# Kernel optimization log

Measured on AMD Instinct MI355X. Metric: run time of the kernel, lower is better.

The kernel has to match this reference:

```python
import jax, jax.numpy as jnp
import numpy as np

D = 1024; NHEAD = 8; NQ = 256; B = 8; HM = 64; WM = 64; S = HM * WM; FF = 4 * D
EPS_LN = 1e-5


def _ln(x, g, b):
    m = x.mean(-1, keepdims=True)
    v = ((x - m) ** 2).mean(-1, keepdims=True)
    return (x - m) / jnp.sqrt(v + EPS_LN) * g + b


def _self_attn(x, w_in, b_in, w_out, b_out, nhead):
    # x: [L, B, D] (torch MultiheadAttention, batch_first=False, eval mode)
    L, Bn, Dm = x.shape
    hd = Dm // nhead
    qkv = x @ w_in.T + b_in  # [L, B, 3D]
    q, k, v = jnp.split(qkv, 3, axis=-1)
    sp = lambda t: t.reshape(L, Bn, nhead, hd).transpose(1, 2, 0, 3)  # [B, H, L, hd]
    q, k, v = sp(q), sp(k), sp(v)
    attn = jax.nn.softmax(jnp.einsum('bhqd,bhkd->bhqk', q, k) / float(hd) ** 0.5, axis=-1)
    out = jnp.einsum('bhqk,bhkd->bhqd', attn, v)
    out = out.transpose(2, 0, 1, 3).reshape(L, Bn, Dm)
    return out @ w_out.T + b_out


def setup_inputs() -> dict:
    key = jax.random.key(0)
    ks = iter(jax.random.split(key, 40))
    nrm = lambda shape: jax.random.normal(next(ks), shape, jnp.float32) * 0.02
    return dict(
        query=jax.random.normal(next(ks), (NQ, B, D), jnp.float32),
        memory=jax.random.normal(next(ks), (S, B, D), jnp.float32),
        prev_mask=jax.random.uniform(next(ks), (B, NQ, HM, WM), dtype=jnp.float32),
        h_mem=HM, w_mem=WM,
        sa_in_w=nrm((3 * D, D)), sa_in_b=jnp.zeros((3 * D,), jnp.float32),
        sa_out_w=nrm((D, D)), sa_out_b=jnp.zeros((D,), jnp.float32),
        ln1_g=jnp.ones((D,), jnp.float32), ln1_b=jnp.zeros((D,), jnp.float32),
        ln2_g=jnp.ones((D,), jnp.float32), ln2_b=jnp.zeros((D,), jnp.float32),
        ln3_g=jnp.ones((D,), jnp.float32), ln3_b=jnp.zeros((D,), jnp.float32),
        wq=nrm((D, D)), bq=jnp.zeros((D,), jnp.float32),
        wk=nrm((D, D)), bk=jnp.zeros((D,), jnp.float32),
        wv=nrm((D, D)), bv=jnp.zeros((D,), jnp.float32),
        wo=nrm((D, D)), bo=jnp.zeros((D,), jnp.float32),
        w1=nrm((FF, D)), b1=jnp.zeros((FF,), jnp.float32),
        w2=nrm((D, FF)), b2=jnp.zeros((D,), jnp.float32),
        mask_w=nrm((S, D)), mask_b=jnp.zeros((S,), jnp.float32),
    )


def reference(query, memory, prev_mask, h_mem, w_mem,
              sa_in_w, sa_in_b, sa_out_w, sa_out_b,
              ln1_g, ln1_b, ln2_g, ln2_b, ln3_g, ln3_b,
              wq, bq, wk, bk, wv, bv, wo, bo,
              w1, b1, w2, b2, mask_w, mask_b):
    nq, Bn, d_model = query.shape
    # --- self attention block ---
    q_norm = _ln(query, ln1_g, ln1_b)
    q2 = _self_attn(q_norm, sa_in_w, sa_in_b, sa_out_w, sa_out_b, NHEAD)
    query = query + q2
    # --- masked cross attention (single-head, as in source) ---
    Q = (_ln(query, ln2_g, ln2_b) @ wq.T + bq).transpose(1, 0, 2)  # [B, NQ, D]
    K = (memory @ wk.T + bk).transpose(1, 0, 2)                    # [B, S, D]
    V = (memory @ wv.T + bv).transpose(1, 0, 2)                    # [B, S, D]
    scores = jnp.einsum('bqd,bsd->bqs', Q, K) / float(d_model) ** 0.5
    scores = scores + jnp.log(prev_mask.reshape(Bn, nq, -1) + 1e-6)
    attn = jax.nn.softmax(scores, axis=-1)
    attn_out = jnp.einsum('bqs,bsd->bqd', attn, V).transpose(1, 0, 2)  # [NQ, B, D]
    query = query + (attn_out @ wo.T + bo)
    # --- FFN ---
    h = jax.nn.gelu(_ln(query, ln3_g, ln3_b) @ w1.T + b1, approximate=False)
    query = query + (h @ w2.T + b2)
    # --- mask prediction ---
    q_for_mask = query.transpose(1, 0, 2)                # [B, NQ, D]
    mask_logits = q_for_mask @ mask_w.T + mask_b          # [B, NQ, H*W]
    pred_mask = jax.nn.sigmoid(mask_logits.reshape(Bn, nq, h_mem, w_mem))
    return (query, pred_mask)
```

## Files before the change

kernel.cpp:

```cpp
#include <hip/hip_runtime.h>
#include <cstdint>


typedef __attribute__((ext_vector_type(8))) __bf16 bf16x8;
typedef __attribute__((ext_vector_type(4))) float f32x4;
typedef __attribute__((ext_vector_type(8))) unsigned short ushort8;
typedef __attribute__((ext_vector_type(4))) unsigned short ushort4v;

__device__ __forceinline__ unsigned short f2bf(float f) {
  return __builtin_bit_cast(unsigned short, (__bf16)f);
}

__global__ __launch_bounds__(256) void cast_bf16_kernel(const float* __restrict__ in,
                                                        unsigned short* __restrict__ out,
                                                        int n8) {
  int i = blockIdx.x * 256 + threadIdx.x;
  if (i >= n8) return;
  const float4* p = (const float4*)in + (size_t)i * 2;
  float4 a = p[0], b = p[1];
  ushort8 o;
  o[0] = f2bf(a.x); o[1] = f2bf(a.y); o[2] = f2bf(a.z); o[3] = f2bf(a.w);
  o[4] = f2bf(b.x); o[5] = f2bf(b.y); o[6] = f2bf(b.z); o[7] = f2bf(b.w);
  ((ushort8*)out)[i] = o;
}

struct CastSegs {
  const float* src[9];
  int cum[10];
};
__global__ __launch_bounds__(256) void cast_multi_kernel(CastSegs cs,
                                                         unsigned short* __restrict__ out) {
  int i = blockIdx.x * 256 + threadIdx.x;
  if (i >= cs.cum[9]) return;
  int s = 0;
  while (i >= cs.cum[s + 1]) s++;
  const float4* p = (const float4*)cs.src[s] + (size_t)(i - cs.cum[s]) * 2;
  float4 a = p[0], b = p[1];
  ushort8 o;
  o[0] = f2bf(a.x); o[1] = f2bf(a.y); o[2] = f2bf(a.z); o[3] = f2bf(a.w);
  o[4] = f2bf(b.x); o[5] = f2bf(b.y); o[6] = f2bf(b.z); o[7] = f2bf(b.w);
  ((ushort8*)out)[i] = o;
}

__global__ __launch_bounds__(256) void bias_concat_kernel(const float* __restrict__ a,
                                                          const float* __restrict__ b,
                                                          float* __restrict__ o) {
  int i = blockIdx.x * 256 + threadIdx.x;
  o[i] = i < 1024 ? a[i] : b[i - 1024];
}

__global__ __launch_bounds__(256) void ln_bf16_kernel(const float* __restrict__ x,
                                                      const float* __restrict__ g,
                                                      const float* __restrict__ b,
                                                      unsigned short* __restrict__ out) {
  int row = blockIdx.x, tid = threadIdx.x;
  const float4* xr = (const float4*)(x + (size_t)row * 1024);
  float4 v = xr[tid];
  float s = v.x + v.y + v.z + v.w;
  float sq = v.x * v.x + v.y * v.y + v.z * v.z + v.w * v.w;
#pragma unroll
  for (int o = 32; o > 0; o >>= 1) { s += __shfl_xor(s, o); sq += __shfl_xor(sq, o); }
  __shared__ float red[8];
  int wave = tid >> 6, lane = tid & 63;
  if (lane == 0) { red[wave] = s; red[4 + wave] = sq; }
  __syncthreads();
  float ts = red[0] + red[1] + red[2] + red[3];
  float tq = red[4] + red[5] + red[6] + red[7];
  float mean = ts * (1.f / 1024.f);
  float var = tq * (1.f / 1024.f) - mean * mean;
  float rstd = rsqrtf(var + 1e-5f);
  float4 gv = ((const float4*)g)[tid];
  float4 bv = ((const float4*)b)[tid];
  ushort4v o;
  o[0] = f2bf((v.x - mean) * rstd * gv.x + bv.x);
  o[1] = f2bf((v.y - mean) * rstd * gv.y + bv.y);
  o[2] = f2bf((v.z - mean) * rstd * gv.z + bv.z);
  o[3] = f2bf((v.w - mean) * rstd * gv.w + bv.w);
  ((ushort4v*)(out + (size_t)row * 1024))[tid] = o;
}

template <bool MASK, int CNT>
__global__ __launch_bounds__(256) void softmax_bf16_kernel(const float* __restrict__ sc,
                                                           const float* __restrict__ pm,
                                                           unsigned short* __restrict__ out,
                                                           float scale) {
  const int L = CNT * 256;
  int row = blockIdx.x, tid = threadIdx.x;
  const float* sr = sc + (size_t)row * L;
  float vals[CNT];
  float mx = -1e30f;
#pragma unroll
  for (int i = 0; i < CNT; i++) {
    int idx = tid + (i << 8);
    float v = sr[idx] * scale;
    if (MASK) v += __logf(pm[(size_t)row * L + idx] + 1e-6f);
    vals[i] = v;
    mx = fmaxf(mx, v);
  }
#pragma unroll
  for (int o = 32; o > 0; o >>= 1) mx = fmaxf(mx, __shfl_xor(mx, o));
  __shared__ float red[8];
  int wave = tid >> 6, lane = tid & 63;
  if (lane == 0) red[wave] = mx;
  __syncthreads();
  mx = fmaxf(fmaxf(red[0], red[1]), fmaxf(red[2], red[3]));
  float sum = 0.f;
#pragma unroll
  for (int i = 0; i < CNT; i++) { vals[i] = __expf(vals[i] - mx); sum += vals[i]; }
#pragma unroll
  for (int o = 32; o > 0; o >>= 1) sum += __shfl_xor(sum, o);
  if (lane == 0) red[4 + wave] = sum;
  __syncthreads();
  float rs = 1.f / (red[4] + red[5] + red[6] + red[7]);
#pragma unroll
  for (int i = 0; i < CNT; i++)
    out[(size_t)row * L + tid + (i << 8)] = f2bf(vals[i] * rs);
}

__global__ __launch_bounds__(256) void transpose_bf16_kernel(
    const unsigned short* __restrict__ in, unsigned short* __restrict__ out,
    long in_off, int in_rs, long in_hi, long in_lo, int zdiv,
    long out_off, int out_rs, long out_hi, long out_lo) {
  __shared__ unsigned short t[32][33];
  int z = blockIdx.z;
  int zh = z / zdiv, zl = z % zdiv;
  const unsigned short* ib = in + in_off + (long)zh * in_hi + (long)zl * in_lo;
  unsigned short* ob = out + out_off + (long)zh * out_hi + (long)zl * out_lo;
  int i0 = blockIdx.x * 32;
  int j0 = blockIdx.y * 32;
  int tx = threadIdx.x & 31, ty = threadIdx.x >> 5;
#pragma unroll
  for (int r = ty; r < 32; r += 8) t[r][tx] = ib[(long)(j0 + r) * in_rs + i0 + tx];
  __syncthreads();
#pragma unroll
  for (int r = ty; r < 32; r += 8) ob[(long)(i0 + r) * out_rs + j0 + tx] = t[tx][r];
}

template <int TM, bool AF32, bool BIAS, int ACT, bool RES, bool OUTF, bool OUTB, bool KVSPLIT>
__global__ __launch_bounds__(256) void gemm_nt_kernel(
    const void* __restrict__ Av, long a_off, int lda, long a_hi, long a_lo,
    const unsigned short* __restrict__ B, long b_off, int ldb, long b_hi, long b_lo,
    const float* __restrict__ bias, const float* __restrict__ Res,
    float* __restrict__ Cf, long c_off, int ldc, long c_hi, long c_lo,
    unsigned short* __restrict__ Cb, long cb_off, int ldcb, long cb_hi, long cb_lo,
    int K, int zdiv) {
  constexpr int MI = TM / 32;
  __shared__ unsigned short As[2 * TM * 32];
  __shared__ unsigned short Bs[2 * 128 * 32];
  int tid = threadIdx.x;
  int wave = tid >> 6, lane = tid & 63;
  int z = blockIdx.z, zh = z / zdiv, zl = z % zdiv;
  long m0 = (long)blockIdx.x * TM, n0 = (long)blockIdx.y * 128;

  const unsigned short* Bb = B + b_off + zh * b_hi + zl * b_lo + n0 * ldb;
  const unsigned short* Ab16 = nullptr;
  const float* Abf = nullptr;
  if constexpr (AF32)
    Abf = (const float*)Av + a_off + zh * a_hi + zl * a_lo + m0 * lda;
  else
    Ab16 = (const unsigned short*)Av + a_off + zh * a_hi + zl * a_lo + m0 * lda;

  int srow = lane >> 2;
  int scol = (lane & 3) * 8;
  int wm = (wave >> 1) * (TM / 2), wn = (wave & 1) * 64;
  int fr = lane & 15;
  int ko = (lane >> 4) * 8;

  f32x4 acc[MI][4] = {};

  auto stage = [&](int buf, int k0) {
    unsigned short* Ad = As + buf * (TM * 32);
    unsigned short* Bd = Bs + buf * (128 * 32);
    if constexpr (AF32) {
      int row = tid >> 1;
      int cs = (tid & 1) * 16;
      const float* ap = Abf + (long)row * lda + k0 + cs;
      float4 f0 = ((const float4*)ap)[0];
      float4 f1 = ((const float4*)ap)[1];
      float4 f2 = ((const float4*)ap)[2];
      float4 f3 = ((const float4*)ap)[3];
      ushort8 u0, u1;
      u0[0] = f2bf(f0.x); u0[1] = f2bf(f0.y); u0[2] = f2bf(f0.z); u0[3] = f2bf(f0.w);
      u0[4] = f2bf(f1.x); u0[5] = f2bf(f1.y); u0[6] = f2bf(f1.z); u0[7] = f2bf(f1.w);
      u1[0] = f2bf(f2.x); u1[1] = f2bf(f2.y); u1[2] = f2bf(f2.z); u1[3] = f2bf(f2.w);
      u1[4] = f2bf(f3.x); u1[5] = f2bf(f3.y); u1[6] = f2bf(f3.z); u1[7] = f2bf(f3.w);
      ushort8* dst = (ushort8*)(Ad + row * 32 + cs);
      dst[0] = u0;
      dst[1] = u1;
    } else {
#pragma unroll
      for (int is = 0; is < TM / 64; is++) {
        int rbase = wave * (TM / 4) + is * 16;
        const unsigned short* g = Ab16 + (long)(rbase + srow) * lda + k0 + scol;
        __builtin_amdgcn_global_load_lds(
            (const __attribute__((address_space(1))) unsigned int*)g,
            (__attribute__((address_space(3))) unsigned int*)(Ad + rbase * 32), 16, 0, 0);
      }
    }
#pragma unroll
    for (int is = 0; is < 2; is++) {
      int rbase = wave * 32 + is * 16;
      const unsigned short* g = Bb + (long)(rbase + srow) * ldb + k0 + scol;
      __builtin_amdgcn_global_load_lds(
          (const __attribute__((address_space(1))) unsigned int*)g,
          (__attribute__((address_space(3))) unsigned int*)(Bd + rbase * 32), 16, 0, 0);
    }
  };

  stage(0, 0);
  int cur = 0;
  for (int k0 = 0; k0 < K; k0 += 32, cur ^= 1) {
    __syncthreads();
    if (k0 + 32 < K) stage(cur ^ 1, k0 + 32);

    const unsigned short* Ar = As + cur * (TM * 32);
    const unsigned short* Br = Bs + cur * (128 * 32);
    bf16x8 af[MI], bfv[4];
#pragma unroll
    for (int i = 0; i < MI; i++)
      af[i] = *(const bf16x8*)(Ar + (wm + i * 16 + fr) * 32 + ko);
#pragma unroll
    for (int j = 0; j < 4; j++)
      bfv[j] = *(const bf16x8*)(Br + (wn + j * 16 + fr) * 32 + ko);
#pragma unroll
    for (int i = 0; i < MI; i++)
#pragma unroll
      for (int j = 0; j < 4; j++)
        acc[i][j] = __builtin_amdgcn_mfma_f32_16x16x32_bf16(af[i], bfv[j], acc[i][j], 0, 0, 0);
  }

  long cfo = c_off + zh * c_hi + zl * c_lo;
  long cbo = cb_off + zh * cb_hi + zl * cb_lo;
  int rq = (lane >> 4) * 4;
#pragma unroll
  for (int i = 0; i < MI; i++) {
    long rbase = m0 + wm + i * 16 + rq;
#pragma unroll
    for (int j = 0; j < 4; j++) {
      long cc = n0 + wn + j * 16 + fr;
      float bsv = BIAS ? bias[cc] : 0.f;
      long p = KVSPLIT ? ((cc >> 10) * cb_hi + (cc & 1023)) : cc;
#pragma unroll
      for (int r = 0; r < 4; r++) {
        float v = acc[i][j][r] + bsv;
        long ro = rbase + r;
        if constexpr (RES) v += Res[cfo + ro * ldc + cc];
        if constexpr (ACT == 1) v = 0.5f * v * (1.f + erff(v * 0.7071067811865475f));
        if constexpr (ACT == 2) v = 1.f / (1.f + __expf(-v));
        if constexpr (OUTF) Cf[cfo + ro * ldc + cc] = v;
        if constexpr (OUTB) Cb[cbo + ro * ldcb + p] = f2bf(v);
      }
    }
  }
}

#define KV_TILE(T, AFA, BFV, AFAN, BFVN, VM1, LG2, DOSTAGE, DONEXT)            \
  {                                                                            \
    const unsigned short* Abuf = &lds[(T) & 3][0][0];                          \
    const unsigned short* AbufN = &lds[((T) + 1) & 3][0][0];                   \
    const unsigned short* BbufN = &lds[((T) + 1) & 3][1][0];                   \
    _Pragma("unroll") for (int i = 0; i < 4; i++)                              \
        afB[i] = *(const bf16x8*)(Abuf + aoff + 2048 + i * 512);               \
    if (DOSTAGE) stageA(((T) + 3) & 3, ((T) + 3) * 32);                        \
    __builtin_amdgcn_sched_barrier(0);                                         \
    asm volatile("s_waitcnt lgkmcnt(4)" ::: "memory");                         \
    __builtin_amdgcn_sched_barrier(0);                                         \
    __builtin_amdgcn_s_setprio(1);                                             \
    _Pragma("unroll") for (int i = 0; i < 4; i++)                              \
        _Pragma("unroll") for (int n = 0; n < 4; n++)                          \
            acc[i][n] = __builtin_amdgcn_mfma_f32_16x16x32_bf16(               \
                AFA[i], BFV[n], acc[i][n], 0, 0, 0);                           \
    __builtin_amdgcn_s_setprio(0);                                             \
    asm volatile("s_waitcnt vmcnt(" #VM1 ")" ::: "memory");                    \
    __builtin_amdgcn_s_barrier();                                              \
    if (DONEXT) {                                                              \
      _Pragma("unroll") for (int i = 0; i < 4; i++)                            \
          AFAN[i] = *(const bf16x8*)(AbufN + aoff + i * 512);                  \
      _Pragma("unroll") for (int n = 0; n < 4; n++)                            \
          BFVN[n] = *(const bf16x8*)(BbufN + boff + n * 512);                  \
    }                                                                          \
    if (DOSTAGE) stageB(((T) + 3) & 3, ((T) + 3) * 32);                        \
    __builtin_amdgcn_sched_barrier(0);                                         \
    asm volatile("s_waitcnt lgkmcnt(" #LG2 ")" ::: "memory");                  \
    __builtin_amdgcn_sched_barrier(0);                                         \
    __builtin_amdgcn_s_setprio(1);                                             \
    _Pragma("unroll") for (int i = 0; i < 4; i++)                              \
        _Pragma("unroll") for (int n = 0; n < 4; n++)                          \
            acc[4 + i][n] = __builtin_amdgcn_mfma_f32_16x16x32_bf16(           \
                afB[i], BFV[n], acc[4 + i][n], 0, 0, 0);                       \
    __builtin_amdgcn_s_setprio(0);                                             \
    __builtin_amdgcn_s_barrier();                                              \
  }

__global__ __launch_bounds__(512) void gemm256_kv_kernel(
    const unsigned short* __restrict__ A,
    const unsigned short* __restrict__ B,
    const float* __restrict__ bias,
    unsigned short* __restrict__ C,
    long plane) {
  __shared__ __align__(1024) unsigned short lds[4][2][8192];
  const int K = 1024, NT = 32;
  int tid = threadIdx.x;
  int wave = tid >> 6, lane = tid & 63;
  int wr = wave >> 2, wc = wave & 3;
  int fr = lane & 15, hi = lane >> 4;

  int l = blockIdx.x >> 3;
  long m0 = (long)((blockIdx.x & 7) * 16 + (l >> 3)) * 256;
  int n0 = (l & 7) * 256;

  const unsigned short* Ab = A + m0 * K;
  const unsigned short* Bb = B + (long)n0 * K;

  int lr = lane >> 2;
  int lc = (((lane & 3) ^ ((lane >> 5) << 1)) << 3);

  auto stageA = [&](int buf, int k0) {
    const unsigned short* g0 = Ab + (long)(wave * 16 + lr) * K + k0 + lc;
    __builtin_amdgcn_global_load_lds(
        (const __attribute__((address_space(1))) unsigned int*)g0,
        (__attribute__((address_space(3))) unsigned int*)&lds[buf][0][wave * 512], 16, 0, 0);
    const unsigned short* g1 = g0 + (long)128 * K;
    __builtin_amdgcn_global_load_lds(
        (const __attribute__((address_space(1))) unsigned int*)g1,
        (__attribute__((address_space(3))) unsigned int*)&lds[buf][0][4096 + wave * 512], 16, 0, 0);
  };
  auto stageB = [&](int buf, int k0) {
    const unsigned short* g0 = Bb + (long)(wave * 16 + lr) * K + k0 + lc;
    __builtin_amdgcn_global_load_lds(
        (const __attribute__((address_space(1))) unsigned int*)g0,
        (__attribute__((address_space(3))) unsigned int*)&lds[buf][1][wave * 512], 16, 0, 0);
    const unsigned short* g1 = g0 + (long)128 * K;
    __builtin_amdgcn_global_load_lds(
        (const __attribute__((address_space(1))) unsigned int*)g1,
        (__attribute__((address_space(3))) unsigned int*)&lds[buf][1][4096 + wave * 512], 16, 0, 0);
  };

  int cbel = ((hi * 16) ^ ((fr >> 3) << 5)) >> 1;
  int aoff = (wr * 128 + fr) * 32 + cbel;
  int boff = (wc * 64 + fr) * 32 + cbel;

  f32x4 acc[8][4] = {};
  bf16x8 afA_p[4], bfv_p[4], afA_q[4], bfv_q[4], afB[4];

#pragma unroll
  for (int t = 0; t < 3; t++) { stageA(t, t * 32); stageB(t, t * 32); }
  asm volatile("s_waitcnt vmcnt(8)" ::: "memory");
  __builtin_amdgcn_s_barrier();
  {
    const unsigned short* Abuf0 = &lds[0][0][0];
    const unsigned short* Bbuf0 = &lds[0][1][0];
#pragma unroll
    for (int i = 0; i < 4; i++) afA_p[i] = *(const bf16x8*)(Abuf0 + aoff + i * 512);
#pragma unroll
    for (int n = 0; n < 4; n++) bfv_p[n] = *(const bf16x8*)(Bbuf0 + boff + n * 512);
  }

  for (int t = 0; t < 28; t += 2) {
    KV_TILE(t, afA_p, bfv_p, afA_q, bfv_q, 6, 8, 1, 1)
    KV_TILE(t + 1, afA_q, bfv_q, afA_p, bfv_p, 6, 8, 1, 1)
  }
  KV_TILE(28, afA_p, bfv_p, afA_q, bfv_q, 6, 8, 1, 1)
  KV_TILE(29, afA_q, bfv_q, afA_p, bfv_p, 4, 8, 0, 1)
  KV_TILE(30, afA_p, bfv_p, afA_q, bfv_q, 0, 8, 0, 1)
  KV_TILE(31, afA_q, bfv_q, afA_p, bfv_p, 0, 0, 0, 0)

  int rq = hi * 4;
#pragma unroll
  for (int i = 0; i < 8; i++) {
    long r0 = m0 + wr * 128 + i * 16 + rq;
#pragma unroll
    for (int n = 0; n < 4; n++) {
      int cc = n0 + wc * 64 + n * 16 + fr;
      float bsv = bias[cc];
      long p = (long)(cc >> 10) * plane + (cc & 1023);
#pragma unroll
      for (int r = 0; r < 4; r++)
        C[p + (r0 + r) * 1024] = f2bf(acc[i][n][r] + bsv);
    }
  }
}

template <int TM, bool AF32, bool BIAS, int ACT, bool RES, bool OUTF, bool OUTB, bool KVSPLIT = false>
static void launch_gemm(hipStream_t s, int M, int N, int K, int nz, int zdiv,
                        const void* A, long a_off, int lda, long a_hi, long a_lo,
                        const unsigned short* B, long b_off, int ldb, long b_hi, long b_lo,
                        const float* bias, const float* Res,
                        float* Cf, long c_off, int ldc, long c_hi, long c_lo,
                        unsigned short* Cb, long cb_off, int ldcb, long cb_hi, long cb_lo) {
  dim3 g(M / TM, N / 128, nz);
  gemm_nt_kernel<TM, AF32, BIAS, ACT, RES, OUTF, OUTB, KVSPLIT><<<g, dim3(256), 0, s>>>(
      A, a_off, lda, a_hi, a_lo, B, b_off, ldb, b_hi, b_lo, bias, Res,
      Cf, c_off, ldc, c_hi, c_lo, Cb, cb_off, ldcb, cb_hi, cb_lo, K, zdiv);
}

static const long WB_SAIN = 0;
static const long WB_SAOUT = 6291456;
static const long WB_WQ = 8388608;
static const long WB_WK = 10485760;
static const long WB_WV = 12582912;
static const long WB_WO = 14680064;
static const long WB_W1 = 16777216;
static const long WB_W2 = 25165824;
static const long WB_MW = 33554432;
static const long OF_K = 41943040;
static const long OF_V = 109051904;
static const long OF_QKV = 176160768;
static const long OF_BKV = 187695104;
static const long OF_SC = 188743680;
static const long OF_P = 222298112;
static const long OF_QN = 239075328;
static const long OF_Q = 243269632;
static const long OF_CTX = 247463936;
static const long OF_MEMBF = 251658240;
static const size_t FAST_WS = 318767104;

extern "C" void kernel_launch(void* const* d_in, const int* in_sizes, int n_in,
                              void* d_out, int out_size, void* d_ws, size_t ws_size,
                              hipStream_t stream) {
  (void)in_sizes; (void)n_in; (void)out_size;
  const float* query = (const float*)d_in[0];
  const float* memoryp = (const float*)d_in[1];
  const float* prev_mask = (const float*)d_in[2];
  const float* sa_in_w = (const float*)d_in[5];
  const float* sa_in_b = (const float*)d_in[6];
  const float* sa_out_w = (const float*)d_in[7];
  const float* sa_out_b = (const float*)d_in[8];
  const float* ln1_g = (const float*)d_in[9], * ln1_b = (const float*)d_in[10];
  const float* ln2_g = (const float*)d_in[11], * ln2_b = (const float*)d_in[12];
  const float* ln3_g = (const float*)d_in[13], * ln3_b = (const float*)d_in[14];
  const float* wq = (const float*)d_in[15], * bq = (const float*)d_in[16];
  const float* wk = (const float*)d_in[17], * bk = (const float*)d_in[18];
  const float* wv = (const float*)d_in[19], * bv = (const float*)d_in[20];
  const float* wo = (const float*)d_in[21], * bo = (const float*)d_in[22];
  const float* w1 = (const float*)d_in[23], * b1 = (const float*)d_in[24];
  const float* w2 = (const float*)d_in[25], * b2 = (const float*)d_in[26];
  const float* mask_w = (const float*)d_in[27], * mask_b = (const float*)d_in[28];

  uint8_t* ws = (uint8_t*)d_ws;
  auto bf = [&](long off) { return (unsigned short*)(ws + off); };
  auto fp = [&](long off) { return (float*)(ws + off); };
  unsigned short* ZB = nullptr;
  float* ZF = nullptr;
  const bool fast = ws_size >= FAST_WS;

  {
    CastSegs cs;
    const float* srcs[9] = {sa_in_w, sa_out_w, wq, wk, wv, wo, w1, w2, mask_w};
    int n8s[9] = {393216, 131072, 131072, 131072, 131072, 131072, 524288, 524288, 524288};
    int c = 0;
    for (int i = 0; i < 9; i++) { cs.src[i] = srcs[i]; cs.cum[i] = c; c += n8s[i]; }
    cs.cum[9] = c;
    cast_multi_kernel<<<dim3((c + 255) / 256), dim3(256), 0, stream>>>(cs, bf(0));
  }

  ln_bf16_kernel<<<2048, 256, 0, stream>>>(query, ln1_g, ln1_b, bf(OF_QN));

  launch_gemm<128, false, true, 0, false, false, true>(stream, 2048, 3072, 1024, 1, 1,
      bf(OF_QN), 0, 1024, 0, 0, bf(WB_SAIN), 0, 1024, 0, 0, sa_in_b, nullptr,
      ZF, 0, 0, 0, 0, bf(OF_QKV), 0, 3072, 0, 0);

  launch_gemm<128, false, false, 0, false, true, false>(stream, 256, 256, 128, 64, 8,
      bf(OF_QKV), 0, 24576, 3072, 128,
      bf(OF_QKV), 1024, 24576, 3072, 128, nullptr, nullptr,
      fp(OF_SC), 0, 256, 524288, 65536, ZB, 0, 0, 0, 0);

  softmax_bf16_kernel<false, 1><<<16384, 256, 0, stream>>>(
      fp(OF_SC), nullptr, bf(OF_P), 0.08838834764831845f);

  transpose_bf16_kernel<<<dim3(4, 8, 64), 256, 0, stream>>>(
      bf(OF_QKV), bf(OF_QN), 2048L, 24576, 3072L, 128L, 8, 0L, 256, 262144L, 32768L);

  launch_gemm<64, false, false, 0, false, false, true>(stream, 256, 128, 256, 64, 8,
      bf(OF_P), 0, 256, 524288, 65536,
      bf(OF_QN), 0, 256, 262144, 32768, nullptr, nullptr,
      ZF, 0, 0, 0, 0, bf(OF_CTX), 0, 8192, 1024, 128);

  launch_gemm<64, false, true, 0, true, true, false>(stream, 2048, 1024, 1024, 1, 1,
      bf(OF_CTX), 0, 1024, 0, 0, bf(WB_SAOUT), 0, 1024, 0, 0, sa_out_b, query,
      fp(OF_QKV), 0, 1024, 0, 0, ZB, 0, 0, 0, 0);

  ln_bf16_kernel<<<2048, 256, 0, stream>>>(fp(OF_QKV), ln2_g, ln2_b, bf(OF_QN));

  launch_gemm<64, false, true, 0, false, false, true>(stream, 2048, 1024, 1024, 1, 1,
      bf(OF_QN), 0, 1024, 0, 0, bf(WB_WQ), 0, 1024, 0, 0, bq, nullptr,
      ZF, 0, 0, 0, 0, bf(OF_Q), 0, 1024, 0, 0);

  bias_concat_kernel<<<8, 256, 0, stream>>>(bk, bv, fp(OF_BKV));
  if (fast) {
    cast_bf16_kernel<<<16384, 256, 0, stream>>>(memoryp, bf(OF_MEMBF), 4194304);
    gemm256_kv_kernel<<<dim3(1024), dim3(512), 0, stream>>>(
        bf(OF_MEMBF), bf(WB_WK), fp(OF_BKV), bf(OF_K), 33554432L);
  } else {
    launch_gemm<128, true, true, 0, false, false, true, true>(stream, 32768, 2048, 1024, 1, 1,
        memoryp, 0, 1024, 0, 0, bf(WB_WK), 0, 1024, 0, 0, fp(OF_BKV), nullptr,
        ZF, 0, 0, 0, 0, bf(OF_K), 0, 1024, 33554432, 0);
  }

  launch_gemm<128, false, false, 0, false, true, false>(stream, 256, 4096, 1024, 8, 1,
      bf(OF_Q), 0, 8192, 1024, 0,
      bf(OF_K), 0, 8192, 1024, 0, nullptr, nullptr,
      fp(OF_SC), 0, 4096, 1048576, 0, ZB, 0, 0, 0, 0);

  softmax_bf16_kernel<true, 16><<<2048, 256, 0, stream>>>(
      fp(OF_SC), prev_mask, bf(OF_P), 0.03125f);

  transpose_bf16_kernel<<<dim3(32, 128, 8), 256, 0, stream>>>(
      bf(OF_V), bf(OF_K), 0L, 8192, 1024L, 0L, 1, 0L, 4096, 4194304L, 0L);

  launch_gemm<64, false, false, 0, false, false, true>(stream, 256, 1024, 4096, 8, 1,
      bf(OF_P), 0, 4096, 1048576, 0,
      bf(OF_K), 0, 4096, 4194304, 0, nullptr, nullptr,
      ZF, 0, 0, 0, 0, bf(OF_CTX), 0, 8192, 1024, 0);

  launch_gemm<64, false, true, 0, true, true, false>(stream, 2048, 1024, 1024, 1, 1,
      bf(OF_CTX), 0, 1024, 0, 0, bf(WB_WO), 0, 1024, 0, 0, bo, fp(OF_QKV),
      fp(OF_SC), 0, 1024, 0, 0, ZB, 0, 0, 0, 0);

  ln_bf16_kernel<<<2048, 256, 0, stream>>>(fp(OF_SC), ln3_g, ln3_b, bf(OF_QN));

  launch_gemm<128, false, true, 1, false, false, true>(stream, 2048, 4096, 1024, 1, 1,
      bf(OF_QN), 0, 1024, 0, 0, bf(WB_W1), 0, 1024, 0, 0, b1, nullptr,
      ZF, 0, 0, 0, 0, bf(OF_P), 0, 4096, 0, 0);

  launch_gemm<64, false, true, 0, true, true, true>(stream, 2048, 1024, 4096, 1, 1,
      bf(OF_P), 0, 4096, 0, 0, bf(WB_W2), 0, 4096, 0, 0, b2, fp(OF_SC),
      (float*)d_out, 0, 1024, 0, 0, bf(OF_CTX), 0, 1024, 0, 0);

  launch_gemm<128, false, true, 2, false, true, false>(stream, 256, 4096, 1024, 8, 1,
      bf(OF_CTX), 0, 8192, 1024, 0,
      bf(WB_MW), 0, 1024, 0, 0, mask_b, nullptr,
      (float*)d_out + 2097152, 0, 4096, 1048576, 0, ZB, 0, 0, 0, 0);
}
```

Baseline: 944.0 us.

## Retile KV GEMM to 256x128 blocks with 4 waves and triple-buffered LDS

Reshapes the K/V projection GEMM from 512-thread 256x256 tiles with a 4-stage LDS ring to 256-thread 256x128 tiles with a 3-stage ring, doubling the grid. Each wave now issues all A and B global-to-LDS loads for a stage together, with a prefetch distance of two. The smaller LDS footprint should allow more blocks per CU and better latency hiding. The cost is more re-reading of the activation matrix across N tiles and a shallower prefetch.

```diff
diff --git a/kernel.cpp b/kernel.cpp
--- a/kernel.cpp
+++ b/kernel.cpp
@@ -254,14 +254,36 @@
   }
 }
 
+#define KV_STAGE(BUFL, K0)                                                     \
+  {                                                                            \
+    __builtin_amdgcn_global_load_lds(                                          \
+        (const __attribute__((address_space(1))) unsigned int*)(gA0 + (K0)),   \
+        (__attribute__((address_space(3))) unsigned int*)&ldsA[BUFL][wave * 2048 + 0], 16, 0, 0); \
+    __builtin_amdgcn_global_load_lds(                                          \
+        (const __attribute__((address_space(1))) unsigned int*)(gA1 + (K0)),   \
+        (__attribute__((address_space(3))) unsigned int*)&ldsA[BUFL][wave * 2048 + 512], 16, 0, 0); \
+    __builtin_amdgcn_global_load_lds(                                          \
+        (const __attribute__((address_space(1))) unsigned int*)(gA2 + (K0)),   \
+        (__attribute__((address_space(3))) unsigned int*)&ldsA[BUFL][wave * 2048 + 1024], 16, 0, 0); \
+    __builtin_amdgcn_global_load_lds(                                          \
+        (const __attribute__((address_space(1))) unsigned int*)(gA3 + (K0)),   \
+        (__attribute__((address_space(3))) unsigned int*)&ldsA[BUFL][wave * 2048 + 1536], 16, 0, 0); \
+    __builtin_amdgcn_global_load_lds(                                          \
+        (const __attribute__((address_space(1))) unsigned int*)(gB0 + (K0)),   \
+        (__attribute__((address_space(3))) unsigned int*)&ldsB[BUFL][wave * 1024 + 0], 16, 0, 0); \
+    __builtin_amdgcn_global_load_lds(                                          \
+        (const __attribute__((address_space(1))) unsigned int*)(gB1 + (K0)),   \
+        (__attribute__((address_space(3))) unsigned int*)&ldsB[BUFL][wave * 1024 + 512], 16, 0, 0); \
+  }
+
 #define KV_TILE(T, AFA, BFV, AFAN, BFVN, VM1, LG2, DOSTAGE, DONEXT)            \
   {                                                                            \
-    const unsigned short* Abuf = &lds[(T) & 3][0][0];                          \
-    const unsigned short* AbufN = &lds[((T) + 1) & 3][0][0];                   \
-    const unsigned short* BbufN = &lds[((T) + 1) & 3][1][0];                   \
+    const unsigned short* Ac = &ldsA[(T) % 3][0];                              \
+    const unsigned short* An = &ldsA[((T) + 1) % 3][0];                        \
+    const unsigned short* Bn = &ldsB[((T) + 1) % 3][0];                        \
     _Pragma("unroll") for (int i = 0; i < 4; i++)                              \
-        afB[i] = *(const bf16x8*)(Abuf + aoff + 2048 + i * 512);               \
-    if (DOSTAGE) stageA(((T) + 3) & 3, ((T) + 3) * 32);                        \
+        afB[i] = *(const bf16x8*)(Ac + aoff + 2048 + i * 512);                 \
+    if (DOSTAGE) KV_STAGE(((T) + 2) % 3, ((T) + 2) * 32)                       \
     __builtin_amdgcn_sched_barrier(0);                                         \
     asm volatile("s_waitcnt lgkmcnt(4)" ::: "memory");                         \
     __builtin_amdgcn_sched_barrier(0);                                         \
@@ -275,11 +297,10 @@
     __builtin_amdgcn_s_barrier();                                              \
     if (DONEXT) {                                                              \
       _Pragma("unroll") for (int i = 0; i < 4; i++)                            \
-          AFAN[i] = *(const bf16x8*)(AbufN + aoff + i * 512);                  \
+          AFAN[i] = *(const bf16x8*)(An + aoff + i * 512);                     \
       _Pragma("unroll") for (int n = 0; n < 4; n++)                            \
-          BFVN[n] = *(const bf16x8*)(BbufN + boff + n * 512);                  \
+          BFVN[n] = *(const bf16x8*)(Bn + boff + n * 512);                     \
     }                                                                          \
-    if (DOSTAGE) stageB(((T) + 3) & 3, ((T) + 3) * 32);                        \
     __builtin_amdgcn_sched_barrier(0);                                         \
     asm volatile("s_waitcnt lgkmcnt(" #LG2 ")" ::: "memory");                  \
     __builtin_amdgcn_sched_barrier(0);                                         \
@@ -292,49 +313,35 @@
     __builtin_amdgcn_s_barrier();                                              \
   }
 
-__global__ __launch_bounds__(512) void gemm256_kv_kernel(
+__global__ __launch_bounds__(256) void gemm256_kv_kernel(
     const unsigned short* __restrict__ A,
     const unsigned short* __restrict__ B,
     const float* __restrict__ bias,
     unsigned short* __restrict__ C,
     long plane) {
-  __shared__ __align__(1024) unsigned short lds[4][2][8192];
-  const int K = 1024, NT = 32;
+  __shared__ __align__(1024) unsigned short ldsA[3][8192];
+  __shared__ __align__(1024) unsigned short ldsB[3][4096];
   int tid = threadIdx.x;
   int wave = tid >> 6, lane = tid & 63;
-  int wr = wave >> 2, wc = wave & 3;
+  int wr = wave >> 1, wc = wave & 1;
   int fr = lane & 15, hi = lane >> 4;
 
   int l = blockIdx.x >> 3;
-  long m0 = (long)((blockIdx.x & 7) * 16 + (l >> 3)) * 256;
-  int n0 = (l & 7) * 256;
-
-  const unsigned short* Ab = A + m0 * K;
-  const unsigned short* Bb = B + (long)n0 * K;
+  long m0 = (long)((blockIdx.x & 7) * 16 + (l >> 4)) * 256;
+  int n0 = (l & 15) * 128;
+
+  const unsigned short* Ab = A + m0 * 1024;
+  const unsigned short* Bb = B + (long)n0 * 1024;
 
   int lr = lane >> 2;
   int lc = (((lane & 3) ^ ((lane >> 5) << 1)) << 3);
 
-  auto stageA = [&](int buf, int k0) {
-    const unsigned short* g0 = Ab + (long)(wave * 16 + lr) * K + k0 + lc;
-    __builtin_amdgcn_global_load_lds(
-        (const __attribute__((address_space(1))) unsigned int*)g0,
-        (__attribute__((address_space(3))) unsigned int*)&lds[buf][0][wave * 512], 16, 0, 0);
-    const unsigned short* g1 = g0 + (long)128 * K;
-    __builtin_amdgcn_global_load_lds(
-        (const __attribute__((address_space(1))) unsigned int*)g1,
-        (__attribute__((address_space(3))) unsigned int*)&lds[buf][0][4096 + wave * 512], 16, 0, 0);
-  };
-  auto stageB = [&](int buf, int k0) {
-    const unsigned short* g0 = Bb + (long)(wave * 16 + lr) * K + k0 + lc;
-    __builtin_amdgcn_global_load_lds(
-        (const __attribute__((address_space(1))) unsigned int*)g0,
-        (__attribute__((address_space(3))) unsigned int*)&lds[buf][1][wave * 512], 16, 0, 0);
-    const unsigned short* g1 = g0 + (long)128 * K;
-    __builtin_amdgcn_global_load_lds(
-        (const __attribute__((address_space(1))) unsigned int*)g1,
-        (__attribute__((address_space(3))) unsigned int*)&lds[buf][1][4096 + wave * 512], 16, 0, 0);
-  };
+  const unsigned short* gA0 = Ab + (long)(wave * 64 + 0 + lr) * 1024 + lc;
+  const unsigned short* gA1 = Ab + (long)(wave * 64 + 16 + lr) * 1024 + lc;
+  const unsigned short* gA2 = Ab + (long)(wave * 64 + 32 + lr) * 1024 + lc;
+  const unsigned short* gA3 = Ab + (long)(wave * 64 + 48 + lr) * 1024 + lc;
+  const unsigned short* gB0 = Bb + (long)(wave * 32 + 0 + lr) * 1024 + lc;
+  const unsigned short* gB1 = Bb + (long)(wave * 32 + 16 + lr) * 1024 + lc;
 
   int cbel = ((hi * 16) ^ ((fr >> 3) << 5)) >> 1;
   int aoff = (wr * 128 + fr) * 32 + cbel;
@@ -343,17 +350,17 @@
   f32x4 acc[8][4] = {};
   bf16x8 afA_p[4], bfv_p[4], afA_q[4], bfv_q[4], afB[4];
 
-#pragma unroll
-  for (int t = 0; t < 3; t++) { stageA(t, t * 32); stageB(t, t * 32); }
-  asm volatile("s_waitcnt vmcnt(8)" ::: "memory");
+  KV_STAGE(0, 0)
+  KV_STAGE(1, 32)
+  asm volatile("s_waitcnt vmcnt(6)" ::: "memory");
   __builtin_amdgcn_s_barrier();
   {
-    const unsigned short* Abuf0 = &lds[0][0][0];
-    const unsigned short* Bbuf0 = &lds[0][1][0];
-#pragma unroll
-    for (int i = 0; i < 4; i++) afA_p[i] = *(const bf16x8*)(Abuf0 + aoff + i * 512);
-#pragma unroll
-    for (int n = 0; n < 4; n++) bfv_p[n] = *(const bf16x8*)(Bbuf0 + boff + n * 512);
+    const unsigned short* A0 = &ldsA[0][0];
+    const unsigned short* B0 = &ldsB[0][0];
+#pragma unroll
+    for (int i = 0; i < 4; i++) afA_p[i] = *(const bf16x8*)(A0 + aoff + i * 512);
+#pragma unroll
+    for (int n = 0; n < 4; n++) bfv_p[n] = *(const bf16x8*)(B0 + boff + n * 512);
   }
 
   for (int t = 0; t < 28; t += 2) {
@@ -361,7 +368,7 @@
     KV_TILE(t + 1, afA_q, bfv_q, afA_p, bfv_p, 6, 8, 1, 1)
   }
   KV_TILE(28, afA_p, bfv_p, afA_q, bfv_q, 6, 8, 1, 1)
-  KV_TILE(29, afA_q, bfv_q, afA_p, bfv_p, 4, 8, 0, 1)
+  KV_TILE(29, afA_q, bfv_q, afA_p, bfv_p, 6, 8, 1, 1)
   KV_TILE(30, afA_p, bfv_p, afA_q, bfv_q, 0, 8, 0, 1)
   KV_TILE(31, afA_q, bfv_q, afA_p, bfv_p, 0, 0, 0, 0)
 
@@ -489,7 +496,7 @@
   bias_concat_kernel<<<8, 256, 0, stream>>>(bk, bv, fp(OF_BKV));
   if (fast) {
     cast_bf16_kernel<<<16384, 256, 0, stream>>>(memoryp, bf(OF_MEMBF), 4194304);
-    gemm256_kv_kernel<<<dim3(1024), dim3(512), 0, stream>>>(
+    gemm256_kv_kernel<<<dim3(2048), dim3(256), 0, stream>>>(
         bf(OF_MEMBF), bf(WB_WK), fp(OF_BKV), bf(OF_K), 33554432L);
   } else {
     launch_gemm<128, true, true, 0, false, false, true, true>(stream, 32768, 2048, 1024, 1, 1,
```

Measured after the change: 1.067 ms. 13.0% more time.
